# Kernel tuning notes

Measured on AMD Instinct MI355X. Metric: run time of the kernel, lower is better.

## Reference

```python
import jax, jax.numpy as jnp
import numpy as np

jax.config.update("jax_enable_x64", True)

B, S = 256, 256
TINY = float(np.finfo(np.float64).tiny)  # torch.finfo().tiny for double


def _matrix_tree_logZ(scores, mask):
    """scores: [B,S,S] float64, mask: [B,S] bool (col 0 is False).
    Returns sum over batch of log partition function (Matrix-Tree theorem)."""
    lens = mask.sum(-1)  # token counts per sentence (excludes root col)
    mask_r = mask.at[:, 0].set(True)  # index_fill(1, 0, 1)
    pair = mask_r[:, :, None] & mask_r[:, None, :]  # [B,S,S]
    s = jnp.where(pair, scores, -jnp.inf)
    m = jnp.max(s.reshape(s.shape[0], -1), axis=-1)  # [B] per-batch max for stability
    A = jnp.maximum(jnp.exp(s - m[:, None, None]), TINY)  # clamp like torch
    idx = jnp.arange(S)
    D = jnp.zeros_like(A).at[:, idx, idx].set(A.sum(-1))  # degree matrix
    eye = jnp.eye(S, dtype=A.dtype)
    # masked_scatter_: rows with mask_r True take (D - A) rows, else identity
    L = jnp.where(mask_r[:, :, None], D - A, eye)
    logZ = jnp.linalg.slogdet(L[:, 1:, 1:])[1] + m * lens
    return logZ.sum()


def setup_inputs() -> dict:
    key = jax.random.key(0)
    k1, k2 = jax.random.split(key)
    scores = jax.random.normal(k1, (B, S, S), dtype=jnp.float32)
    lens = jax.random.randint(k2, (B,), S // 2, S)  # sentence lengths
    pos = jnp.arange(S)
    # col 0 (pseudo root) False, padding beyond length False
    mask = (pos[None, :] >= 1) & (pos[None, :] < lens[:, None])
    return {"scores": scores, "mask": mask}


def reference(scores, mask):
    # mbr=True path: marginals = d logZ / d scores (computed in double like torch)
    s64 = scores.astype(jnp.float64)
    probs = jax.grad(_matrix_tree_logZ)(s64, mask)
    return probs.astype(jnp.float32)
```

## Files before the change

kernel.cpp:

```cpp
#include <hip/hip_runtime.h>
#include <math.h>


#define S 256
#define BB 256

__device__ __forceinline__ int rowmap(int lr, int kb) {
    int rt = lr >> 6;
    int rb = rt + (rt >= kb ? 1 : 0);
    return rb * 64 + (lr & 63);
}

__global__ void k_reduce(const float* __restrict__ sc, const unsigned char* __restrict__ mk,
                         double* __restrict__ mb, int* __restrict__ nb) {
    int b = blockIdx.x, j = threadIdx.x;
    __shared__ int shc[4];
    __shared__ double shm[4];
    __shared__ int shn;

    const unsigned int* mw = (const unsigned int*)mk;
    unsigned int w0 = mw[0], w1 = mw[1];
    int mode = (w0 != 0u) ? 0 : ((w1 != 0u) ? 1 : 2);

    int c;
    if (mode == 0)      c = (mk[(size_t)b * S + j] != 0);
    else if (mode == 1) c = (((const int*)mk)[(size_t)b * S + j] != 0);
    else                c = (((const long long*)mk)[(size_t)b * S + j] != 0LL);

    int lane = j & 63, wid = j >> 6;
    int cs = c;
    for (int off = 32; off > 0; off >>= 1) cs += __shfl_down(cs, off);
    if (lane == 0) shc[wid] = cs;
    __syncthreads();
    if (j == 0) shn = shc[0] + shc[1] + shc[2] + shc[3];
    __syncthreads();
    int n = shn;

    double lm = -1.0e300;
    if (j <= n) {
        for (int i = 0; i <= n; ++i)
            lm = fmax(lm, (double)sc[((size_t)b * S + i) * S + j]);
    }
    for (int off = 32; off > 0; off >>= 1) lm = fmax(lm, __shfl_down(lm, off));
    if (lane == 0) shm[wid] = lm;
    __syncthreads();
    if (j == 0) {
        mb[b] = fmax(fmax(shm[0], shm[1]), fmax(shm[2], shm[3]));
        nb[b] = n;
    }
}

__global__ void k_build(const float* __restrict__ sc, const double* __restrict__ mb,
                        const int* __restrict__ nb, double* __restrict__ Mg) {
    int p = blockIdx.x, b = blockIdx.y, j = threadIdx.x;
    int n = nb[b];
    double* Mrow = Mg + ((size_t)b * S + p) * S;
    if (p >= n) {
        Mrow[j] = (j == p) ? 1.0 : 0.0;
        return;
    }
    __shared__ double se[S];
    __shared__ double shs[4];
    double m = mb[b];
    double e = (j <= n) ? (double)expf((float)((double)sc[((size_t)b * S + (p + 1)) * S + j] - m)) : 0.0;
    se[j] = e;
    int lane = j & 63, wid = j >> 6;
    double ssum = e;
    for (int off = 32; off > 0; off >>= 1) ssum += __shfl_down(ssum, off);
    if (lane == 0) shs[wid] = ssum;
    __syncthreads();
    double rowsum = shs[0] + shs[1] + shs[2] + shs[3];
    double v;
    if (j < n) v = ((j == p) ? rowsum : 0.0) - se[j + 1];
    else       v = (j == p) ? 1.0 : 0.0;
    Mrow[j] = v;
}

__global__ __launch_bounds__(256) void k_gjreg(double* __restrict__ Mg, double* __restrict__ Pg,
                                               int kb) {
    int b = blockIdx.x, tid = threadIdx.x;
    double* M = Mg + (size_t)b * S * S;
    double* P = Pg + (size_t)b * 4096;
    __shared__ double rowbuf[64];
    __shared__ double colbuf[64];

    int i = tid >> 2, g = tid & 3, c0 = g << 4;
    double c[16];
    #pragma unroll
    for (int u = 0; u < 16; ++u)
        c[u] = M[(size_t)(kb * 64 + i) * S + kb * 64 + c0 + u];

    for (int kt = 0; kt < 4; ++kt) {
        #pragma unroll
        for (int ks = 0; ks < 16; ++ks) {
            int k = kt * 16 + ks;
            if (i == k) {
                #pragma unroll
                for (int u = 0; u < 16; ++u) rowbuf[c0 + u] = c[u];
            }
            if (g == kt) colbuf[i] = c[ks];
            __syncthreads();
            double pv = rowbuf[k];
            double f  = colbuf[i];
            double pivinv = 1.0 / pv;
            double rk[16];
            #pragma unroll
            for (int m2 = 0; m2 < 8; ++m2) {
                double2 t = *(const double2*)&rowbuf[c0 + 2 * m2];
                rk[2 * m2] = t.x; rk[2 * m2 + 1] = t.y;
            }
            if (i == k) {
                #pragma unroll
                for (int u = 0; u < 16; ++u)
                    c[u] = ((g == kt) && (u == ks)) ? pivinv : c[u] * pivinv;
            } else {
                double gm = f * pivinv;
                #pragma unroll
                for (int u = 0; u < 16; ++u)
                    c[u] = ((g == kt) && (u == ks)) ? (-gm) : fma(-gm, rk[u], c[u]);
            }
            __syncthreads();
        }
    }
    #pragma unroll
    for (int u = 0; u < 16; ++u) {
        P[i * 64 + c0 + u] = c[u];
        M[(size_t)(kb * 64 + i) * S + kb * 64 + c0 + u] = c[u];
    }
}

__global__ __launch_bounds__(256) void k_rowG(double* __restrict__ Mg,
                                              const double* __restrict__ Pg, int kb) {
    int b = blockIdx.x, tid = threadIdx.x;
    double* M = Mg + (size_t)b * S * S;
    const double* P = Pg + (size_t)b * 4096;
    __shared__ double PT[64][66];
    __shared__ double Rs[64][200];
    {
        int cidx = tid & 63;
        #pragma unroll
        for (int rep = 0; rep < 16; ++rep) {
            int r = rep * 4 + (tid >> 6);
            PT[cidx][r] = P[r * 64 + cidx];
            int s = r;
            #pragma unroll
            for (int cc = 0; cc < 3; ++cc) {
                int j = cc * 64 + cidx;
                Rs[s][j] = M[(size_t)(kb * 64 + s) * S + rowmap(j, kb)];
            }
        }
    }
    __syncthreads();
    int tx = tid & 15, ty = tid >> 4;
    double2 acc[4][6];
    #pragma unroll
    for (int q = 0; q < 4; ++q)
        #pragma unroll
        for (int w = 0; w < 6; ++w) acc[q][w] = double2{0.0, 0.0};

    for (int s = 0; s < 64; ++s) {
        double2 p01 = *(const double2*)&PT[s][4 * ty];
        double2 p23 = *(const double2*)&PT[s][4 * ty + 2];
        #pragma unroll
        for (int w = 0; w < 6; ++w) {
            double2 r = *(const double2*)&Rs[s][2 * tx + 32 * w];
            acc[0][w].x = fma(p01.x, r.x, acc[0][w].x); acc[0][w].y = fma(p01.x, r.y, acc[0][w].y);
            acc[1][w].x = fma(p01.y, r.x, acc[1][w].x); acc[1][w].y = fma(p01.y, r.y, acc[1][w].y);
            acc[2][w].x = fma(p23.x, r.x, acc[2][w].x); acc[2][w].y = fma(p23.x, r.y, acc[2][w].y);
            acc[3][w].x = fma(p23.y, r.x, acc[3][w].x); acc[3][w].y = fma(p23.y, r.y, acc[3][w].y);
        }
    }
    #pragma unroll
    for (int q = 0; q < 4; ++q) {
        size_t row = (size_t)(kb * 64 + 4 * ty + q) * S;
        #pragma unroll
        for (int w = 0; w < 6; ++w) {
            int j = 2 * tx + 32 * w;
            *(double2*)&M[row + rowmap(j, kb)] = acc[q][w];
        }
    }
}

__global__ __launch_bounds__(256) void k_int(double* __restrict__ Mg, int kb) {
    int id = blockIdx.x;
    int b = id >> 1, half = id & 1;
    double* M = Mg + (size_t)b * S * S;
    int tid = threadIdx.x;
    __shared__ double FTs[32][98];
    __shared__ double Rss[32][200];

    int tx = tid & 15, ty = tid >> 4;
    double2 acc[6][6];
    #pragma unroll
    for (int q = 0; q < 6; ++q)
        #pragma unroll
        for (int w = 0; w < 6; ++w) acc[q][w] = double2{0.0, 0.0};

    for (int ck = 0; ck < 2; ++ck) {
        __syncthreads();
        {
            int kk = tid & 31, lrb = (tid >> 5) * 12;
            #pragma unroll
            for (int q = 0; q < 12; ++q) {
                int lrg = half * 96 + lrb + q;
                FTs[kk][lrb + q] =
                    M[(size_t)rowmap(lrg, kb) * S + kb * 64 + ck * 32 + kk];
            }
            int jl = tid & 63, ss = tid >> 6;
            #pragma unroll
            for (int rep = 0; rep < 8; ++rep) {
                int kk2 = ss + 4 * rep;
                #pragma unroll
                for (int cc = 0; cc < 3; ++cc) {
                    int j = cc * 64 + jl;
                    Rss[kk2][j] = M[(size_t)(kb * 64 + ck * 32 + kk2) * S + rowmap(j, kb)];
                }
            }
        }
        __syncthreads();
        for (int kk = 0; kk < 32; ++kk) {
            double2 f01 = *(const double2*)&FTs[kk][6 * ty];
            double2 f23 = *(const double2*)&FTs[kk][6 * ty + 2];
            double2 f45 = *(const double2*)&FTs[kk][6 * ty + 4];
            #pragma unroll
            for (int w = 0; w < 6; ++w) {
                double2 r = *(const double2*)&Rss[kk][2 * tx + 32 * w];
                acc[0][w].x = fma(f01.x, r.x, acc[0][w].x); acc[0][w].y = fma(f01.x, r.y, acc[0][w].y);
                acc[1][w].x = fma(f01.y, r.x, acc[1][w].x); acc[1][w].y = fma(f01.y, r.y, acc[1][w].y);
                acc[2][w].x = fma(f23.x, r.x, acc[2][w].x); acc[2][w].y = fma(f23.x, r.y, acc[2][w].y);
                acc[3][w].x = fma(f23.y, r.x, acc[3][w].x); acc[3][w].y = fma(f23.y, r.y, acc[3][w].y);
                acc[4][w].x = fma(f45.x, r.x, acc[4][w].x); acc[4][w].y = fma(f45.x, r.y, acc[4][w].y);
                acc[5][w].x = fma(f45.y, r.x, acc[5][w].x); acc[5][w].y = fma(f45.y, r.y, acc[5][w].y);
            }
        }
    }
    #pragma unroll
    for (int q = 0; q < 6; ++q) {
        int lrg = half * 96 + ty * 6 + q;
        size_t row = (size_t)rowmap(lrg, kb) * S;
        #pragma unroll
        for (int w = 0; w < 6; ++w) {
            int j = 2 * tx + 32 * w;
            double* p = &M[row + rowmap(j, kb)];
            double2 old = *(double2*)p;
            *(double2*)p = double2{old.x - acc[q][w].x, old.y - acc[q][w].y};
        }
    }
}

__global__ __launch_bounds__(256) void k_colP(double* __restrict__ Mg,
                                              const double* __restrict__ Pg, int kb) {
    int b = blockIdx.x, tid = threadIdx.x;
    double* M = Mg + (size_t)b * S * S;
    const double* P = Pg + (size_t)b * 4096;
    __shared__ double FT2[64][194];
    __shared__ double Ps[64][66];
    {
        int k = tid & 63;
        #pragma unroll
        for (int rep = 0; rep < 48; ++rep) {
            int lr = rep * 4 + (tid >> 6);
            FT2[k][lr] = M[(size_t)rowmap(lr, kb) * S + kb * 64 + k];
        }
        #pragma unroll
        for (int rep = 0; rep < 16; ++rep) {
            int r = rep * 4 + (tid >> 6);
            Ps[r][k] = P[r * 64 + k];
        }
    }
    __syncthreads();
    int tx = tid & 15, ty = tid >> 4;
    double2 acc[12][2];
    #pragma unroll
    for (int q = 0; q < 12; ++q) { acc[q][0] = double2{0.0, 0.0}; acc[q][1] = double2{0.0, 0.0}; }

    for (int k = 0; k < 64; ++k) {
        double2 f[6];
        #pragma unroll
        for (int h = 0; h < 6; ++h) f[h] = *(const double2*)&FT2[k][12 * ty + 2 * h];
        double2 r0 = *(const double2*)&Ps[k][2 * tx];
        double2 r1 = *(const double2*)&Ps[k][2 * tx + 32];
        #pragma unroll
        for (int h = 0; h < 6; ++h) {
            acc[2 * h][0].x     = fma(f[h].x, r0.x, acc[2 * h][0].x);
            acc[2 * h][0].y     = fma(f[h].x, r0.y, acc[2 * h][0].y);
            acc[2 * h][1].x     = fma(f[h].x, r1.x, acc[2 * h][1].x);
            acc[2 * h][1].y     = fma(f[h].x, r1.y, acc[2 * h][1].y);
            acc[2 * h + 1][0].x = fma(f[h].y, r0.x, acc[2 * h + 1][0].x);
            acc[2 * h + 1][0].y = fma(f[h].y, r0.y, acc[2 * h + 1][0].y);
            acc[2 * h + 1][1].x = fma(f[h].y, r1.x, acc[2 * h + 1][1].x);
            acc[2 * h + 1][1].y = fma(f[h].y, r1.y, acc[2 * h + 1][1].y);
        }
    }
    #pragma unroll
    for (int q = 0; q < 12; ++q) {
        int lr = ty * 12 + q;
        size_t row = (size_t)rowmap(lr, kb) * S + kb * 64;
        #pragma unroll
        for (int w = 0; w < 2; ++w) {
            int u = 2 * tx + 32 * w;
            *(double2*)&M[row + u] = double2{-acc[q][w].x, -acc[q][w].y};
        }
    }
}

__global__ __launch_bounds__(256) void k_epi(const float* __restrict__ sc,
                                             const double* __restrict__ Mg,
                                             const double* __restrict__ mb,
                                             const int* __restrict__ nb,
                                             float* __restrict__ out) {
    int b = blockIdx.y;
    int t = blockIdx.x;
    int jj = t & 3, ii = t >> 2;
    int tid = threadIdx.x;
    int n = nb[b];
    double m = mb[b];
    const double* X = Mg + (size_t)b * S * S;
    __shared__ double Xs[64][33];
    __shared__ double sdiag[32];
    if (tid < 32) {
        int idx = 32 * ii + tid - 1;
        sdiag[tid] = (idx >= 0) ? X[(size_t)idx * S + idx] : 0.0;
    }
    {
        int c = tid >> 2, a0 = (tid & 3) << 3;
        int xr = 64 * jj + c - 1;
        #pragma unroll
        for (int u = 0; u < 8; ++u) {
            int a = a0 + u;
            int xc = 32 * ii + a - 1;
            Xs[c][a] = (xr >= 0 && xc >= 0) ? X[(size_t)xr * S + xc] : 0.0;
        }
    }
    __syncthreads();
    int cl = tid & 63, ag = tid >> 6;
    #pragma unroll
    for (int aa = 0; aa < 8; ++aa) {
        int a = ag * 8 + aa;
        int i = 32 * ii + a;
        int j = 64 * jj + cl;
        float v = 0.0f;
        if (i >= 1 && i <= n && j <= n) {
            double A = (double)expf((float)((double)sc[((size_t)b * S + i) * S + j] - m));
            double sub = (j >= 1) ? Xs[cl][a] : 0.0;
            v = (float)(A * (sdiag[a] - sub));
        }
        out[((size_t)b * S + i) * S + j] = v;
    }
}

extern "C" void kernel_launch(void* const* d_in, const int* in_sizes, int n_in,
                              void* d_out, int out_size, void* d_ws, size_t ws_size,
                              hipStream_t stream) {
    (void)in_sizes; (void)n_in; (void)out_size; (void)ws_size;
    const float* sc = (const float*)d_in[0];
    const unsigned char* mk = (const unsigned char*)d_in[1];
    double* ws = (double*)d_ws;

    double* M  = ws;
    double* P  = M + (size_t)BB * S * S;
    double* mb = P + (size_t)BB * 4096;
    int*    nb = (int*)(mb + BB);
    float*  out = (float*)d_out;

    k_reduce<<<BB, 256, 0, stream>>>(sc, mk, mb, nb);
    k_build<<<dim3(S, BB), 256, 0, stream>>>(sc, mb, nb, M);
    for (int kb = 0; kb < 4; ++kb) {
        k_gjreg<<<BB, 256, 0, stream>>>(M, P, kb);
        k_rowG<<<BB, 256, 0, stream>>>(M, P, kb);
        k_int<<<2 * BB, 256, 0, stream>>>(M, kb);
        k_colP<<<BB, 256, 0, stream>>>(M, P, kb);
    }
    k_epi<<<dim3(32, BB), 256, 0, stream>>>(sc, M, mb, nb, out);
}
```

Before: 662.5 us.

## Parallelize score max reduction and fuse pivot-block inversion with row update

The per-batch max is now computed by 8 blocks per batch over the whole score matrix using float4 loads. A small kernel then combines the partial maxes and counts mask lengths, replacing the old serial per-column loop. The Gauss-Jordan pivot-block kernel and the row-panel GEMM kernel are merged into one, so the inverted pivot block goes straight into shared memory instead of being reloaded from global memory, and one launch per block step is removed. The max now also covers masked-out entries, which shifts the stabilizing constant. That is harmless mathematically but could change underflow and clamp behaviour.

```diff
diff --git a/kernel.cpp b/kernel.cpp
--- a/kernel.cpp
+++ b/kernel.cpp
@@ -11,12 +11,29 @@
     return rb * 64 + (lr & 63);
 }
 
-__global__ void k_reduce(const float* __restrict__ sc, const unsigned char* __restrict__ mk,
-                         double* __restrict__ mb, int* __restrict__ nb) {
+__global__ __launch_bounds__(256) void k_max(const float* __restrict__ sc,
+                                             float* __restrict__ partial) {
+    int b = blockIdx.y, rg = blockIdx.x;
+    const float4* p4 = (const float4*)(sc + (size_t)b * S * S + rg * 8192);
+    int tid = threadIdx.x;
+    float4 v[8];
+    #pragma unroll
+    for (int it = 0; it < 8; ++it) v[it] = p4[tid + 256 * it];
+    float m = -1e30f;
+    #pragma unroll
+    for (int it = 0; it < 8; ++it)
+        m = fmaxf(m, fmaxf(fmaxf(v[it].x, v[it].y), fmaxf(v[it].z, v[it].w)));
+    for (int off = 32; off > 0; off >>= 1) m = fmaxf(m, __shfl_down(m, off));
+    __shared__ float sm[4];
+    if ((tid & 63) == 0) sm[tid >> 6] = m;
+    __syncthreads();
+    if (tid == 0) partial[b * 8 + rg] = fmaxf(fmaxf(sm[0], sm[1]), fmaxf(sm[2], sm[3]));
+}
+
+__global__ void k_n(const unsigned char* __restrict__ mk, const float* __restrict__ partial,
+                    double* __restrict__ mb, int* __restrict__ nb) {
     int b = blockIdx.x, j = threadIdx.x;
     __shared__ int shc[4];
-    __shared__ double shm[4];
-    __shared__ int shn;
 
     const unsigned int* mw = (const unsigned int*)mk;
     unsigned int w0 = mw[0], w1 = mw[1];
@@ -32,21 +49,12 @@
     for (int off = 32; off > 0; off >>= 1) cs += __shfl_down(cs, off);
     if (lane == 0) shc[wid] = cs;
     __syncthreads();
-    if (j == 0) shn = shc[0] + shc[1] + shc[2] + shc[3];
-    __syncthreads();
-    int n = shn;
-
-    double lm = -1.0e300;
-    if (j <= n) {
-        for (int i = 0; i <= n; ++i)
-            lm = fmax(lm, (double)sc[((size_t)b * S + i) * S + j]);
-    }
-    for (int off = 32; off > 0; off >>= 1) lm = fmax(lm, __shfl_down(lm, off));
-    if (lane == 0) shm[wid] = lm;
-    __syncthreads();
     if (j == 0) {
-        mb[b] = fmax(fmax(shm[0], shm[1]), fmax(shm[2], shm[3]));
-        nb[b] = n;
+        nb[b] = shc[0] + shc[1] + shc[2] + shc[3];
+        float mm = partial[b * 8];
+        #pragma unroll
+        for (int q = 1; q < 8; ++q) mm = fmaxf(mm, partial[b * 8 + q]);
+        mb[b] = (double)mm;
     }
 }
 
@@ -76,11 +84,13 @@
     Mrow[j] = v;
 }
 
-__global__ __launch_bounds__(256) void k_gjreg(double* __restrict__ Mg, double* __restrict__ Pg,
+__global__ __launch_bounds__(256) void k_gjrow(double* __restrict__ Mg, double* __restrict__ Pg,
                                                int kb) {
     int b = blockIdx.x, tid = threadIdx.x;
     double* M = Mg + (size_t)b * S * S;
     double* P = Pg + (size_t)b * 4096;
+    __shared__ double PT[64][66];
+    __shared__ double Rs[64][200];
     __shared__ double rowbuf[64];
     __shared__ double colbuf[64];
 
@@ -124,33 +134,24 @@
     }
     #pragma unroll
     for (int u = 0; u < 16; ++u) {
+        PT[c0 + u][i] = c[u];
         P[i * 64 + c0 + u] = c[u];
         M[(size_t)(kb * 64 + i) * S + kb * 64 + c0 + u] = c[u];
     }
-}
-
-__global__ __launch_bounds__(256) void k_rowG(double* __restrict__ Mg,
-                                              const double* __restrict__ Pg, int kb) {
-    int b = blockIdx.x, tid = threadIdx.x;
-    double* M = Mg + (size_t)b * S * S;
-    const double* P = Pg + (size_t)b * 4096;
-    __shared__ double PT[64][66];
-    __shared__ double Rs[64][200];
     {
         int cidx = tid & 63;
         #pragma unroll
         for (int rep = 0; rep < 16; ++rep) {
             int r = rep * 4 + (tid >> 6);
-            PT[cidx][r] = P[r * 64 + cidx];
-            int s = r;
             #pragma unroll
             for (int cc = 0; cc < 3; ++cc) {
                 int j = cc * 64 + cidx;
-                Rs[s][j] = M[(size_t)(kb * 64 + s) * S + rowmap(j, kb)];
-            }
-        }
-    }
-    __syncthreads();
+                Rs[r][j] = M[(size_t)(kb * 64 + r) * S + rowmap(j, kb)];
+            }
+        }
+    }
+    __syncthreads();
+
     int tx = tid & 15, ty = tid >> 4;
     double2 acc[4][6];
     #pragma unroll
@@ -361,13 +362,14 @@
     double* P  = M + (size_t)BB * S * S;
     double* mb = P + (size_t)BB * 4096;
     int*    nb = (int*)(mb + BB);
+    float*  partial = (float*)P;
     float*  out = (float*)d_out;
 
-    k_reduce<<<BB, 256, 0, stream>>>(sc, mk, mb, nb);
+    k_max<<<dim3(8, BB), 256, 0, stream>>>(sc, partial);
+    k_n<<<BB, 256, 0, stream>>>(mk, partial, mb, nb);
     k_build<<<dim3(S, BB), 256, 0, stream>>>(sc, mb, nb, M);
     for (int kb = 0; kb < 4; ++kb) {
-        k_gjreg<<<BB, 256, 0, stream>>>(M, P, kb);
-        k_rowG<<<BB, 256, 0, stream>>>(M, P, kb);
+        k_gjrow<<<BB, 256, 0, stream>>>(M, P, kb);
         k_int<<<2 * BB, 256, 0, stream>>>(M, kb);
         k_colP<<<BB, 256, 0, stream>>>(M, P, kb);
     }
```

Result: faster. 600.6 us (-9.3%).
